# Performance work log

Hardware: AMD Instinct MI355X
Metric: run time of the kernel (lower is better)

## Reference

```python
import jax, jax.numpy as jnp
import numpy as np

# normalization module stand-ins (simple monotone scalings, as in the repo they
# are fixed elementwise rescalings of the raw quantities)
def norm_local_x(n):
    return n

def norm_unit_contraction(c):
    return c

def norm_local_N(N):
    return jnp.log1p(N.astype(jnp.float32))

norm_TNG_radii = norm_local_x
norm_local_v = norm_local_x
norm_local_v0 = norm_local_x

EPS = 1e-5


def setup_inputs() -> dict:
    key = jax.random.key(0)
    ks = jax.random.split(key, 12)
    B, T, ND, KB = 2, 1024, 256, 3
    K_IN, H, L = 19, 128, 128
    x0 = 0.3 * jax.random.normal(ks[0], (B, T, 3), dtype=jnp.float32)
    # DM positions in local frame, |x| must stay < 1.05 (assert in original)
    x = jax.random.uniform(ks[1], (B, T, ND, 3), dtype=jnp.float32) - 0.5
    N = jax.random.randint(ks[2], (B, T), 1, 512, dtype=jnp.int32)
    basis = jax.random.normal(ks[3], (B, KB, 3), dtype=jnp.float32)
    v = jax.random.normal(ks[4], (B, T, ND, 3), dtype=jnp.float32)
    P200c = 0.5 + jax.random.uniform(ks[5], (B,), dtype=jnp.float32)
    s = 0.1
    W0 = s * jax.random.normal(ks[6], (K_IN, H - 1), dtype=jnp.float32)
    b0 = jnp.zeros((H - 1,), jnp.float32)
    W1 = s * jax.random.normal(ks[7], (H, H), dtype=jnp.float32)
    b1 = jnp.zeros((H,), jnp.float32)
    W2 = s * jax.random.normal(ks[8], (H, L), dtype=jnp.float32)
    b2 = jnp.zeros((L,), jnp.float32)
    return {"x0": x0, "x": x, "N": N, "basis": basis, "v": v, "P200c": P200c,
            "W0": W0, "b0": b0, "W1": W1, "b1": b1, "W2": W2, "b2": b2}


def create_scalars(x0, x, N, basis, v):
    B, T, ND, _ = x.shape
    # velocities relative to local mean (halo -> local frame)
    v0 = jnp.mean(v, axis=2)                      # [B,T,3]
    vc = v - v0[:, :, None, :]                    # [B,T,ND,3]

    x_norm = jnp.linalg.norm(x, axis=-1, keepdims=True) + EPS     # [B,T,ND,1]
    xu = x / x_norm
    x0_norm = jnp.linalg.norm(x0, axis=-1, keepdims=True) + EPS   # [B,T,1]
    x0u = x0 / x0_norm
    v0_norm = jnp.linalg.norm(v0, axis=-1, keepdims=True) + EPS   # [B,T,1]
    v0u = v0 / v0_norm
    v_norm = jnp.linalg.norm(vc, axis=-1, keepdims=True) + EPS    # [B,T,ND,1]
    vu = vc / v_norm

    bc = lambda a: jnp.broadcast_to(a[:, :, None, :], (B, T, ND, a.shape[-1]))

    feats = [
        norm_local_x(x_norm),                                          # |x| [1]
        norm_unit_contraction(jnp.einsum('btnd,bkd->btnk', xu, basis)),# x.basis [3]
        jnp.broadcast_to(norm_local_N(N)[:, :, None, None], (B, T, ND, 1)),  # N [1]
        bc(norm_TNG_radii(x0_norm)),                                   # |x0| [1]
        bc(norm_unit_contraction(jnp.einsum('btd,bkd->btk', x0u, basis))),  # x0.basis [3]
        bc(norm_local_v0(v0_norm)),                                    # |v0| [1]
        bc(norm_unit_contraction(jnp.einsum('btd,bkd->btk', v0u, basis))),  # v0.basis [3]
        bc(norm_unit_contraction(jnp.sum(x0u * v0u, axis=-1, keepdims=True))),  # x0.v0 [1]
        norm_local_v(v_norm),                                          # |v| [1]
        norm_unit_contraction(jnp.einsum('btnd,bkd->btnk', vu, basis)),# v.basis [3]
        norm_unit_contraction(jnp.sum(xu * vu, axis=-1, keepdims=True)),  # x.v [1]
    ]
    return jnp.concatenate(feats, axis=-1)  # [B,T,ND,19]


def reference(x0, x, N, basis, v, P200c, W0, b0, W1, b1, W2, b2):
    scalars = create_scalars(x0, x, N, basis, v)          # [B,T,ND,19]
    h = jax.nn.leaky_relu(scalars @ W0 + b0)              # [B,T,ND,H-1]
    h = jnp.mean(h, axis=2)                               # pool -> [B,T,H-1]
    h = jnp.concatenate([h, norm_local_N(N)[..., None]], axis=-1)  # [B,T,H]
    h = jax.nn.leaky_relu(h @ W1 + b1)                    # [B,T,H]
    out = h @ W2 + b2                                     # [B,T,Nlatent]
    return (1.0 / P200c)[:, None, None] * out
```

## Files before the change

### kernel.cpp

```cpp
#include <hip/hip_runtime.h>
#include <hip/hip_bf16.h>
#include <math.h>

#define EPSV 1e-5f
#define HD   128
#define AROW 40
#define WROW 24

typedef __attribute__((ext_vector_type(8))) short bf16x8;
typedef __attribute__((ext_vector_type(4))) float f32x4;

__global__ __launch_bounds__(256, 4) void net_fused(
    const float* __restrict__ x0g, const float* __restrict__ xg,
    const int*   __restrict__ Ng,  const float* __restrict__ basisg,
    const float* __restrict__ vg,  const float* __restrict__ Pg,
    const float* __restrict__ W0,  const float* __restrict__ b0,
    const float* __restrict__ W1,  const float* __restrict__ b1,
    const float* __restrict__ W2,  const float* __restrict__ b2,
    float* __restrict__ out, int Tn, int NDn)
{
    __shared__ __align__(16) __hip_bfloat16 SA[256 * AROW];
    __shared__ __align__(16) __hip_bfloat16 Wt1[128 * WROW];
    __shared__ __align__(16) __hip_bfloat16 Wt2[128 * WROW];
    __shared__ float cvec[HD];
    __shared__ float hvec[HD];
    __shared__ float h1vec[HD];
    __shared__ float vred[4][3];

    const int bt   = blockIdx.x;
    const int b    = bt / Tn;
    const int tid  = threadIdx.x;
    const int lane = tid & 63;
    const int wave = tid >> 6;

    const long pbase = ((long)bt * NDn + tid) * 3;
    const float xi0 = xg[pbase+0], xi1 = xg[pbase+1], xi2 = xg[pbase+2];
    const float vi0 = vg[pbase+0], vi1 = vg[pbase+1], vi2 = vg[pbase+2];

    float s0 = vi0, s1 = vi1, s2 = vi2;
    #pragma unroll
    for (int off = 32; off > 0; off >>= 1) {
        s0 += __shfl_down(s0, off);
        s1 += __shfl_down(s1, off);
        s2 += __shfl_down(s2, off);
    }
    if (lane == 0) { vred[wave][0] = s0; vred[wave][1] = s1; vred[wave][2] = s2; }

    if (tid < 128) {
        const int RV[9] = {0, 1, 2, 3, 14, 15, 16, 17, 18};
        __hip_bfloat16 r1[16], r2[16];
        #pragma unroll
        for (int kk = 0; kk < 16; ++kk) {
            r1[kk] = __float2bfloat16(0.0f);
            r2[kk] = __float2bfloat16(0.0f);
        }
        if (tid < 127) {
            #pragma unroll
            for (int kk = 0; kk < 9; ++kk) {
                const float wv = W0[RV[kk] * 127 + tid];
                const __hip_bfloat16 hi = __float2bfloat16(wv);
                r1[kk] = hi;
                r2[kk] = __float2bfloat16(wv - __bfloat162float(hi));
            }
        }
        bf16x8* d1 = reinterpret_cast<bf16x8*>(&Wt1[tid * WROW]);
        bf16x8* d2 = reinterpret_cast<bf16x8*>(&Wt2[tid * WROW]);
        const bf16x8* s1v = reinterpret_cast<const bf16x8*>(r1);
        const bf16x8* s2v = reinterpret_cast<const bf16x8*>(r2);
        d1[0] = s1v[0]; d1[1] = s1v[1];
        d2[0] = s2v[0]; d2[1] = s2v[1];
    }
    __syncthreads();

    const float inv_nd = 1.0f / (float)NDn;
    const float v00 = (vred[0][0]+vred[1][0]+vred[2][0]+vred[3][0]) * inv_nd;
    const float v01 = (vred[0][1]+vred[1][1]+vred[2][1]+vred[3][1]) * inv_nd;
    const float v02 = (vred[0][2]+vred[1][2]+vred[2][2]+vred[3][2]) * inv_nd;

    const float p0 = x0g[bt*3+0], p1 = x0g[bt*3+1], p2 = x0g[bt*3+2];
    float bas[3][3];
    #pragma unroll
    for (int k = 0; k < 3; ++k)
        #pragma unroll
        for (int c = 0; c < 3; ++c)
            bas[k][c] = basisg[(b*3 + k)*3 + c];

    const float x0n  = sqrtf(p0*p0 + p1*p1 + p2*p2) + EPSV;
    const float ix0n = 1.0f / x0n;
    const float x0u0 = p0*ix0n, x0u1 = p1*ix0n, x0u2 = p2*ix0n;

    const float v0n  = sqrtf(v00*v00 + v01*v01 + v02*v02) + EPSV;
    const float iv0n = 1.0f / v0n;
    const float v0u0 = v00*iv0n, v0u1 = v01*iv0n, v0u2 = v02*iv0n;

    const float logN = log1pf((float)Ng[bt]);

    if (tid < 128) {
        float c = 0.0f;
        if (tid < 127) {
            float fc[10];
            fc[0] = logN;
            fc[1] = x0n;
            fc[2] = x0u0*bas[0][0] + x0u1*bas[0][1] + x0u2*bas[0][2];
            fc[3] = x0u0*bas[1][0] + x0u1*bas[1][1] + x0u2*bas[1][2];
            fc[4] = x0u0*bas[2][0] + x0u1*bas[2][1] + x0u2*bas[2][2];
            fc[5] = v0n;
            fc[6] = v0u0*bas[0][0] + v0u1*bas[0][1] + v0u2*bas[0][2];
            fc[7] = v0u0*bas[1][0] + v0u1*bas[1][1] + v0u2*bas[1][2];
            fc[8] = v0u0*bas[2][0] + v0u1*bas[2][1] + v0u2*bas[2][2];
            fc[9] = x0u0*v0u0 + x0u1*v0u1 + x0u2*v0u2;
            c = b0[tid];
            #pragma unroll
            for (int i = 0; i < 10; ++i)
                c = fmaf(fc[i], W0[(4 + i) * 127 + tid], c);
        }
        cvec[tid] = c;
        hvec[tid] = (tid == 127) ? logN : 0.0f;
    }

    {
        const float xn  = sqrtf(xi0*xi0 + xi1*xi1 + xi2*xi2) + EPSV;
        const float ixn = 1.0f / xn;
        const float xu0 = xi0*ixn, xu1 = xi1*ixn, xu2 = xi2*ixn;

        const float c0 = vi0 - v00, c1 = vi1 - v01, c2 = vi2 - v02;
        const float vn  = sqrtf(c0*c0 + c1*c1 + c2*c2) + EPSV;
        const float ivn = 1.0f / vn;
        const float vu0 = c0*ivn, vu1 = c1*ivn, vu2 = c2*ivn;

        float f[9];
        f[0] = xn;
        f[1] = xu0*bas[0][0] + xu1*bas[0][1] + xu2*bas[0][2];
        f[2] = xu0*bas[1][0] + xu1*bas[1][1] + xu2*bas[1][2];
        f[3] = xu0*bas[2][0] + xu1*bas[2][1] + xu2*bas[2][2];
        f[4] = vn;
        f[5] = vu0*bas[0][0] + vu1*bas[0][1] + vu2*bas[0][2];
        f[6] = vu0*bas[1][0] + vu1*bas[1][1] + vu2*bas[1][2];
        f[7] = vu0*bas[2][0] + vu1*bas[2][1] + vu2*bas[2][2];
        f[8] = xu0*vu0 + xu1*vu1 + xu2*vu2;

        __hip_bfloat16 row[32];
        #pragma unroll
        for (int kk = 0; kk < 32; ++kk) row[kk] = __float2bfloat16(0.0f);
        #pragma unroll
        for (int kk = 0; kk < 9; ++kk) {
            const __hip_bfloat16 hi = __float2bfloat16(f[kk]);
            row[kk]      = hi;
            row[16 + kk] = __float2bfloat16(f[kk] - __bfloat162float(hi));
        }
        bf16x8* dst = reinterpret_cast<bf16x8*>(&SA[tid * AROW]);
        const bf16x8* src = reinterpret_cast<const bf16x8*>(row);
        dst[0] = src[0]; dst[1] = src[1]; dst[2] = src[2]; dst[3] = src[3];
    }
    __syncthreads();

    {
        const int quad = lane >> 4;
        const int lm   = lane & 15;
        const int koff = (quad & 1) * 8;

        bf16x8 bf1[8], bf2[8];
        f32x4  cin[8];
        #pragma unroll
        for (int nt = 0; nt < 8; ++nt) {
            bf1[nt] = *reinterpret_cast<const bf16x8*>(&Wt1[(nt*16 + lm) * WROW + koff]);
            bf2[nt] = *reinterpret_cast<const bf16x8*>(&Wt2[(nt*16 + lm) * WROW + koff]);
            const float cl = cvec[nt*16 + lm];
            cin[nt] = (f32x4){cl, cl, cl, cl};
        }

        float pooled[8];
        #pragma unroll
        for (int nt = 0; nt < 8; ++nt) pooled[nt] = 0.0f;

        #pragma unroll
        for (int mt = 0; mt < 4; ++mt) {
            const bf16x8 af = *reinterpret_cast<const bf16x8*>(
                &SA[(wave*64 + mt*16 + lm) * AROW + quad*8]);
            #pragma unroll
            for (int nt = 0; nt < 8; ++nt) {
                f32x4 acc = __builtin_amdgcn_mfma_f32_16x16x32_bf16(af, bf1[nt], cin[nt], 0, 0, 0);
                acc = __builtin_amdgcn_mfma_f32_16x16x32_bf16(af, bf2[nt], acc, 0, 0, 0);
                #pragma unroll
                for (int r = 0; r < 4; ++r)
                    pooled[nt] += fmaxf(acc[r], 0.01f*acc[r]);
            }
        }
        #pragma unroll
        for (int nt = 0; nt < 8; ++nt) {
            pooled[nt] += __shfl_xor(pooled[nt], 16);
            pooled[nt] += __shfl_xor(pooled[nt], 32);
        }
        if (lane < 16) {
            #pragma unroll
            for (int nt = 0; nt < 8; ++nt) {
                const int n = nt*16 + lane;
                if (n < 127) atomicAdd(&hvec[n], pooled[nt] * inv_nd);
            }
        }
    }
    __syncthreads();

    if (tid < HD) {
        float a = b1[tid];
        #pragma unroll 16
        for (int k = 0; k < HD; ++k)
            a = fmaf(hvec[k], W1[k*HD + tid], a);
        h1vec[tid] = fmaxf(a, 0.01f*a);
    }
    __syncthreads();

    if (tid < HD) {
        float a = b2[tid];
        #pragma unroll 16
        for (int k = 0; k < HD; ++k)
            a = fmaf(h1vec[k], W2[k*HD + tid], a);
        out[(long)bt * HD + tid] = a / Pg[b];
    }
}

extern "C" void kernel_launch(void* const* d_in, const int* in_sizes, int n_in,
                              void* d_out, int out_size, void* d_ws, size_t ws_size,
                              hipStream_t stream) {
    const float* x0    = (const float*)d_in[0];
    const float* x     = (const float*)d_in[1];
    const int*   N     = (const int*)  d_in[2];
    const float* basis = (const float*)d_in[3];
    const float* v     = (const float*)d_in[4];
    const float* P200c = (const float*)d_in[5];
    const float* W0    = (const float*)d_in[6];
    const float* b0    = (const float*)d_in[7];
    const float* W1    = (const float*)d_in[8];
    const float* b1    = (const float*)d_in[9];
    const float* W2    = (const float*)d_in[10];
    const float* b2    = (const float*)d_in[11];
    float* out = (float*)d_out;

    const int B  = in_sizes[5];
    const int T  = in_sizes[2] / B;
    const int ND = in_sizes[1] / (in_sizes[2] * 3);

    hipLaunchKernelGGL(net_fused, dim3(B * T), dim3(256), 0, stream,
                       x0, x, N, basis, v, P200c, W0, b0, W1, b1, W2, b2,
                       out, T, ND);
}
```

Measured before the change: 111.3 us.

## Process two (b,t) items per block and parallelize MLP tail across all threads

Each block now handles two consecutive (b,t) rows and loops over them. The bf16 split of W0 into shared memory is therefore done once per pair instead of once per row. The final two 128x128 dense layers run both rows at once, so all 256 threads work instead of 128. This halves the grid and lengthens the serial chain inside each block, trading per-block setup and idle-thread waste for less block-level parallelism.

```diff
diff --git a/kernel.cpp b/kernel.cpp
--- a/kernel.cpp
+++ b/kernel.cpp
@@ -17,34 +17,23 @@
     const float* __restrict__ W0,  const float* __restrict__ b0,
     const float* __restrict__ W1,  const float* __restrict__ b1,
     const float* __restrict__ W2,  const float* __restrict__ b2,
-    float* __restrict__ out, int Tn, int NDn)
+    float* __restrict__ out, int Tn, int NDn, int BT)
 {
     __shared__ __align__(16) __hip_bfloat16 SA[256 * AROW];
     __shared__ __align__(16) __hip_bfloat16 Wt1[128 * WROW];
     __shared__ __align__(16) __hip_bfloat16 Wt2[128 * WROW];
     __shared__ float cvec[HD];
-    __shared__ float hvec[HD];
-    __shared__ float h1vec[HD];
-    __shared__ float vred[4][3];
-
-    const int bt   = blockIdx.x;
-    const int b    = bt / Tn;
+    __shared__ float hvec2[2][HD];
+    __shared__ float h1vec2[2][HD];
+    __shared__ float vred2[2][4][3];
+
+    const int bt0  = blockIdx.x * 2;
     const int tid  = threadIdx.x;
     const int lane = tid & 63;
     const int wave = tid >> 6;
-
-    const long pbase = ((long)bt * NDn + tid) * 3;
-    const float xi0 = xg[pbase+0], xi1 = xg[pbase+1], xi2 = xg[pbase+2];
-    const float vi0 = vg[pbase+0], vi1 = vg[pbase+1], vi2 = vg[pbase+2];
-
-    float s0 = vi0, s1 = vi1, s2 = vi2;
-    #pragma unroll
-    for (int off = 32; off > 0; off >>= 1) {
-        s0 += __shfl_down(s0, off);
-        s1 += __shfl_down(s1, off);
-        s2 += __shfl_down(s2, off);
-    }
-    if (lane == 0) { vred[wave][0] = s0; vred[wave][1] = s1; vred[wave][2] = s2; }
+    const int quad = lane >> 4;
+    const int lm   = lane & 15;
+    const float inv_nd = 1.0f / (float)NDn;
 
     if (tid < 128) {
         const int RV[9] = {0, 1, 2, 3, 14, 15, 16, 17, 18};
@@ -70,152 +59,172 @@
         d1[0] = s1v[0]; d1[1] = s1v[1];
         d2[0] = s2v[0]; d2[1] = s2v[1];
     }
+
+    for (int h = 0; h < 2; ++h) {
+        const int bt = bt0 + h;
+        const int b  = bt / Tn;
+
+        const long pbase = ((long)bt * NDn + tid) * 3;
+        const float xi0 = xg[pbase+0], xi1 = xg[pbase+1], xi2 = xg[pbase+2];
+        const float vi0 = vg[pbase+0], vi1 = vg[pbase+1], vi2 = vg[pbase+2];
+
+        float s0 = vi0, s1 = vi1, s2 = vi2;
+        #pragma unroll
+        for (int off = 32; off > 0; off >>= 1) {
+            s0 += __shfl_down(s0, off);
+            s1 += __shfl_down(s1, off);
+            s2 += __shfl_down(s2, off);
+        }
+        if (lane == 0) {
+            vred2[h][wave][0] = s0; vred2[h][wave][1] = s1; vred2[h][wave][2] = s2;
+        }
+        __syncthreads();
+
+        const float v00 = (vred2[h][0][0]+vred2[h][1][0]+vred2[h][2][0]+vred2[h][3][0]) * inv_nd;
+        const float v01 = (vred2[h][0][1]+vred2[h][1][1]+vred2[h][2][1]+vred2[h][3][1]) * inv_nd;
+        const float v02 = (vred2[h][0][2]+vred2[h][1][2]+vred2[h][2][2]+vred2[h][3][2]) * inv_nd;
+
+        const float p0 = x0g[bt*3+0], p1 = x0g[bt*3+1], p2 = x0g[bt*3+2];
+        float bas[3][3];
+        #pragma unroll
+        for (int k = 0; k < 3; ++k)
+            #pragma unroll
+            for (int c = 0; c < 3; ++c)
+                bas[k][c] = basisg[(b*3 + k)*3 + c];
+
+        const float x0n  = sqrtf(p0*p0 + p1*p1 + p2*p2) + EPSV;
+        const float ix0n = 1.0f / x0n;
+        const float x0u0 = p0*ix0n, x0u1 = p1*ix0n, x0u2 = p2*ix0n;
+
+        const float v0n  = sqrtf(v00*v00 + v01*v01 + v02*v02) + EPSV;
+        const float iv0n = 1.0f / v0n;
+        const float v0u0 = v00*iv0n, v0u1 = v01*iv0n, v0u2 = v02*iv0n;
+
+        const float logN = log1pf((float)Ng[bt]);
+
+        if (tid < 128) {
+            float c = 0.0f;
+            if (tid < 127) {
+                float fc[10];
+                fc[0] = logN;
+                fc[1] = x0n;
+                fc[2] = x0u0*bas[0][0] + x0u1*bas[0][1] + x0u2*bas[0][2];
+                fc[3] = x0u0*bas[1][0] + x0u1*bas[1][1] + x0u2*bas[1][2];
+                fc[4] = x0u0*bas[2][0] + x0u1*bas[2][1] + x0u2*bas[2][2];
+                fc[5] = v0n;
+                fc[6] = v0u0*bas[0][0] + v0u1*bas[0][1] + v0u2*bas[0][2];
+                fc[7] = v0u0*bas[1][0] + v0u1*bas[1][1] + v0u2*bas[1][2];
+                fc[8] = v0u0*bas[2][0] + v0u1*bas[2][1] + v0u2*bas[2][2];
+                fc[9] = x0u0*v0u0 + x0u1*v0u1 + x0u2*v0u2;
+                c = b0[tid];
+                #pragma unroll
+                for (int i = 0; i < 10; ++i)
+                    c = fmaf(fc[i], W0[(4 + i) * 127 + tid], c);
+            }
+            cvec[tid] = c;
+            hvec2[h][tid] = (tid == 127) ? logN : 0.0f;
+        }
+
+        {
+            const float xn  = sqrtf(xi0*xi0 + xi1*xi1 + xi2*xi2) + EPSV;
+            const float ixn = 1.0f / xn;
+            const float xu0 = xi0*ixn, xu1 = xi1*ixn, xu2 = xi2*ixn;
+
+            const float c0 = vi0 - v00, c1 = vi1 - v01, c2 = vi2 - v02;
+            const float vn  = sqrtf(c0*c0 + c1*c1 + c2*c2) + EPSV;
+            const float ivn = 1.0f / vn;
+            const float vu0 = c0*ivn, vu1 = c1*ivn, vu2 = c2*ivn;
+
+            float f[9];
+            f[0] = xn;
+            f[1] = xu0*bas[0][0] + xu1*bas[0][1] + xu2*bas[0][2];
+            f[2] = xu0*bas[1][0] + xu1*bas[1][1] + xu2*bas[1][2];
+            f[3] = xu0*bas[2][0] + xu1*bas[2][1] + xu2*bas[2][2];
+            f[4] = vn;
+            f[5] = vu0*bas[0][0] + vu1*bas[0][1] + vu2*bas[0][2];
+            f[6] = vu0*bas[1][0] + vu1*bas[1][1] + vu2*bas[1][2];
+            f[7] = vu0*bas[2][0] + vu1*bas[2][1] + vu2*bas[2][2];
+            f[8] = xu0*vu0 + xu1*vu1 + xu2*vu2;
+
+            __hip_bfloat16 row[32];
+            #pragma unroll
+            for (int kk = 0; kk < 32; ++kk) row[kk] = __float2bfloat16(0.0f);
+            #pragma unroll
+            for (int kk = 0; kk < 9; ++kk) {
+                const __hip_bfloat16 hi = __float2bfloat16(f[kk]);
+                row[kk]      = hi;
+                row[16 + kk] = __float2bfloat16(f[kk] - __bfloat162float(hi));
+            }
+            bf16x8* dst = reinterpret_cast<bf16x8*>(&SA[tid * AROW]);
+            const bf16x8* src = reinterpret_cast<const bf16x8*>(row);
+            dst[0] = src[0]; dst[1] = src[1]; dst[2] = src[2]; dst[3] = src[3];
+        }
+        __syncthreads();
+
+        {
+            const int koff = (quad & 1) * 8;
+
+            bf16x8 bf1[8], bf2[8];
+            f32x4  cin[8];
+            #pragma unroll
+            for (int nt = 0; nt < 8; ++nt) {
+                bf1[nt] = *reinterpret_cast<const bf16x8*>(&Wt1[(nt*16 + lm) * WROW + koff]);
+                bf2[nt] = *reinterpret_cast<const bf16x8*>(&Wt2[(nt*16 + lm) * WROW + koff]);
+                const float cl = cvec[nt*16 + lm];
+                cin[nt] = (f32x4){cl, cl, cl, cl};
+            }
+
+            float pooled[8];
+            #pragma unroll
+            for (int nt = 0; nt < 8; ++nt) pooled[nt] = 0.0f;
+
+            #pragma unroll
+            for (int mt = 0; mt < 4; ++mt) {
+                const bf16x8 af = *reinterpret_cast<const bf16x8*>(
+                    &SA[(wave*64 + mt*16 + lm) * AROW + quad*8]);
+                #pragma unroll
+                for (int nt = 0; nt < 8; ++nt) {
+                    f32x4 acc = __builtin_amdgcn_mfma_f32_16x16x32_bf16(af, bf1[nt], cin[nt], 0, 0, 0);
+                    acc = __builtin_amdgcn_mfma_f32_16x16x32_bf16(af, bf2[nt], acc, 0, 0, 0);
+                    #pragma unroll
+                    for (int r = 0; r < 4; ++r)
+                        pooled[nt] += fmaxf(acc[r], 0.01f*acc[r]);
+                }
+            }
+            #pragma unroll
+            for (int nt = 0; nt < 8; ++nt) {
+                pooled[nt] += __shfl_xor(pooled[nt], 16);
+                pooled[nt] += __shfl_xor(pooled[nt], 32);
+            }
+            if (lane < 16) {
+                #pragma unroll
+                for (int nt = 0; nt < 8; ++nt) {
+                    const int n = nt*16 + lane;
+                    if (n < 127) atomicAdd(&hvec2[h][n], pooled[nt] * inv_nd);
+                }
+            }
+        }
+    }
     __syncthreads();
 
-    const float inv_nd = 1.0f / (float)NDn;
-    const float v00 = (vred[0][0]+vred[1][0]+vred[2][0]+vred[3][0]) * inv_nd;
-    const float v01 = (vred[0][1]+vred[1][1]+vred[2][1]+vred[3][1]) * inv_nd;
-    const float v02 = (vred[0][2]+vred[1][2]+vred[2][2]+vred[3][2]) * inv_nd;
-
-    const float p0 = x0g[bt*3+0], p1 = x0g[bt*3+1], p2 = x0g[bt*3+2];
-    float bas[3][3];
-    #pragma unroll
-    for (int k = 0; k < 3; ++k)
-        #pragma unroll
-        for (int c = 0; c < 3; ++c)
-            bas[k][c] = basisg[(b*3 + k)*3 + c];
-
-    const float x0n  = sqrtf(p0*p0 + p1*p1 + p2*p2) + EPSV;
-    const float ix0n = 1.0f / x0n;
-    const float x0u0 = p0*ix0n, x0u1 = p1*ix0n, x0u2 = p2*ix0n;
-
-    const float v0n  = sqrtf(v00*v00 + v01*v01 + v02*v02) + EPSV;
-    const float iv0n = 1.0f / v0n;
-    const float v0u0 = v00*iv0n, v0u1 = v01*iv0n, v0u2 = v02*iv0n;
-
-    const float logN = log1pf((float)Ng[bt]);
-
-    if (tid < 128) {
-        float c = 0.0f;
-        if (tid < 127) {
-            float fc[10];
-            fc[0] = logN;
-            fc[1] = x0n;
-            fc[2] = x0u0*bas[0][0] + x0u1*bas[0][1] + x0u2*bas[0][2];
-            fc[3] = x0u0*bas[1][0] + x0u1*bas[1][1] + x0u2*bas[1][2];
-            fc[4] = x0u0*bas[2][0] + x0u1*bas[2][1] + x0u2*bas[2][2];
-            fc[5] = v0n;
-            fc[6] = v0u0*bas[0][0] + v0u1*bas[0][1] + v0u2*bas[0][2];
-            fc[7] = v0u0*bas[1][0] + v0u1*bas[1][1] + v0u2*bas[1][2];
-            fc[8] = v0u0*bas[2][0] + v0u1*bas[2][1] + v0u2*bas[2][2];
-            fc[9] = x0u0*v0u0 + x0u1*v0u1 + x0u2*v0u2;
-            c = b0[tid];
-            #pragma unroll
-            for (int i = 0; i < 10; ++i)
-                c = fmaf(fc[i], W0[(4 + i) * 127 + tid], c);
-        }
-        cvec[tid] = c;
-        hvec[tid] = (tid == 127) ? logN : 0.0f;
-    }
-
+    const int r  = tid >> 7;
+    const int j  = tid & 127;
     {
-        const float xn  = sqrtf(xi0*xi0 + xi1*xi1 + xi2*xi2) + EPSV;
-        const float ixn = 1.0f / xn;
-        const float xu0 = xi0*ixn, xu1 = xi1*ixn, xu2 = xi2*ixn;
-
-        const float c0 = vi0 - v00, c1 = vi1 - v01, c2 = vi2 - v02;
-        const float vn  = sqrtf(c0*c0 + c1*c1 + c2*c2) + EPSV;
-        const float ivn = 1.0f / vn;
-        const float vu0 = c0*ivn, vu1 = c1*ivn, vu2 = c2*ivn;
-
-        float f[9];
-        f[0] = xn;
-        f[1] = xu0*bas[0][0] + xu1*bas[0][1] + xu2*bas[0][2];
-        f[2] = xu0*bas[1][0] + xu1*bas[1][1] + xu2*bas[1][2];
-        f[3] = xu0*bas[2][0] + xu1*bas[2][1] + xu2*bas[2][2];
-        f[4] = vn;
-        f[5] = vu0*bas[0][0] + vu1*bas[0][1] + vu2*bas[0][2];
-        f[6] = vu0*bas[1][0] + vu1*bas[1][1] + vu2*bas[1][2];
-        f[7] = vu0*bas[2][0] + vu1*bas[2][1] + vu2*bas[2][2];
-        f[8] = xu0*vu0 + xu1*vu1 + xu2*vu2;
-
-        __hip_bfloat16 row[32];
-        #pragma unroll
-        for (int kk = 0; kk < 32; ++kk) row[kk] = __float2bfloat16(0.0f);
-        #pragma unroll
-        for (int kk = 0; kk < 9; ++kk) {
-            const __hip_bfloat16 hi = __float2bfloat16(f[kk]);
-            row[kk]      = hi;
-            row[16 + kk] = __float2bfloat16(f[kk] - __bfloat162float(hi));
-        }
-        bf16x8* dst = reinterpret_cast<bf16x8*>(&SA[tid * AROW]);
-        const bf16x8* src = reinterpret_cast<const bf16x8*>(row);
-        dst[0] = src[0]; dst[1] = src[1]; dst[2] = src[2]; dst[3] = src[3];
-    }
-    __syncthreads();
-
-    {
-        const int quad = lane >> 4;
-        const int lm   = lane & 15;
-        const int koff = (quad & 1) * 8;
-
-        bf16x8 bf1[8], bf2[8];
-        f32x4  cin[8];
-        #pragma unroll
-        for (int nt = 0; nt < 8; ++nt) {
-            bf1[nt] = *reinterpret_cast<const bf16x8*>(&Wt1[(nt*16 + lm) * WROW + koff]);
-            bf2[nt] = *reinterpret_cast<const bf16x8*>(&Wt2[(nt*16 + lm) * WROW + koff]);
-            const float cl = cvec[nt*16 + lm];
-            cin[nt] = (f32x4){cl, cl, cl, cl};
-        }
-
-        float pooled[8];
-        #pragma unroll
-        for (int nt = 0; nt < 8; ++nt) pooled[nt] = 0.0f;
-
-        #pragma unroll
-        for (int mt = 0; mt < 4; ++mt) {
-            const bf16x8 af = *reinterpret_cast<const bf16x8*>(
-                &SA[(wave*64 + mt*16 + lm) * AROW + quad*8]);
-            #pragma unroll
-            for (int nt = 0; nt < 8; ++nt) {
-                f32x4 acc = __builtin_amdgcn_mfma_f32_16x16x32_bf16(af, bf1[nt], cin[nt], 0, 0, 0);
-                acc = __builtin_amdgcn_mfma_f32_16x16x32_bf16(af, bf2[nt], acc, 0, 0, 0);
-                #pragma unroll
-                for (int r = 0; r < 4; ++r)
-                    pooled[nt] += fmaxf(acc[r], 0.01f*acc[r]);
-            }
-        }
-        #pragma unroll
-        for (int nt = 0; nt < 8; ++nt) {
-            pooled[nt] += __shfl_xor(pooled[nt], 16);
-            pooled[nt] += __shfl_xor(pooled[nt], 32);
-        }
-        if (lane < 16) {
-            #pragma unroll
-            for (int nt = 0; nt < 8; ++nt) {
-                const int n = nt*16 + lane;
-                if (n < 127) atomicAdd(&hvec[n], pooled[nt] * inv_nd);
-            }
-        }
-    }
-    __syncthreads();
-
-    if (tid < HD) {
-        float a = b1[tid];
+        float a = b1[j];
         #pragma unroll 16
         for (int k = 0; k < HD; ++k)
-            a = fmaf(hvec[k], W1[k*HD + tid], a);
-        h1vec[tid] = fmaxf(a, 0.01f*a);
+            a = fmaf(hvec2[r][k], W1[k*HD + j], a);
+        h1vec2[r][j] = fmaxf(a, 0.01f*a);
     }
     __syncthreads();
 
-    if (tid < HD) {
-        float a = b2[tid];
+    {
+        const int bt = bt0 + r;
+        float a = b2[j];
         #pragma unroll 16
         for (int k = 0; k < HD; ++k)
-            a = fmaf(h1vec[k], W2[k*HD + tid], a);
-        out[(long)bt * HD + tid] = a / Pg[b];
+            a = fmaf(h1vec2[r][k], W2[k*HD + j], a);
+        out[(long)bt * HD + j] = a / Pg[bt / Tn];
     }
 }
 
@@ -239,8 +248,9 @@
     const int B  = in_sizes[5];
     const int T  = in_sizes[2] / B;
     const int ND = in_sizes[1] / (in_sizes[2] * 3);
-
-    hipLaunchKernelGGL(net_fused, dim3(B * T), dim3(256), 0, stream,
+    const int BT = B * T;
+
+    hipLaunchKernelGGL(net_fused, dim3(BT / 2), dim3(256), 0, stream,
                        x0, x, N, basis, v, P200c, W0, b0, W1, b1, W2, b2,
-                       out, T, ND);
+                       out, T, ND, BT);
 }
```

New measurement: 127.1 us. 1.14x slower.

## Drop activation lo-split, pass features by wave shuffle, fold weight split into K

Applied to the files above, without the earlier changes.

The MLP input features are now converted to a single bf16 each, with no hi/lo residual. They are packed into registers and sent to the MFMA A-operand with wave shuffles, which removes the per-point shared-memory staging array. The W0 hi and lo parts are packed into one shared tile along K, so each 16x16x32 MFMA computes A_hi·(W_hi+W_lo) and the MFMA count is halved. Launch bounds are raised to allow more resident blocks. In exchange, the activation-side bf16 rounding error is no longer corrected, which lowers accuracy against the fp32 reference.

```diff
diff --git a/kernel.cpp b/kernel.cpp
--- a/kernel.cpp
+++ b/kernel.cpp
@@ -4,13 +4,19 @@
 
 #define EPSV 1e-5f
 #define HD   128
-#define AROW 40
-#define WROW 24
+#define WROW 40
 
 typedef __attribute__((ext_vector_type(8))) short bf16x8;
 typedef __attribute__((ext_vector_type(4))) float f32x4;
 
-__global__ __launch_bounds__(256, 4) void net_fused(
+static __device__ __forceinline__ unsigned int bfbits(float x) {
+    __hip_bfloat16 h = __float2bfloat16(x);
+    unsigned short u;
+    __builtin_memcpy(&u, &h, 2);
+    return (unsigned int)u;
+}
+
+__global__ __launch_bounds__(256, 6) void net_fused(
     const float* __restrict__ x0g, const float* __restrict__ xg,
     const int*   __restrict__ Ng,  const float* __restrict__ basisg,
     const float* __restrict__ vg,  const float* __restrict__ Pg,
@@ -19,9 +25,7 @@
     const float* __restrict__ W2,  const float* __restrict__ b2,
     float* __restrict__ out, int Tn, int NDn)
 {
-    __shared__ __align__(16) __hip_bfloat16 SA[256 * AROW];
-    __shared__ __align__(16) __hip_bfloat16 Wt1[128 * WROW];
-    __shared__ __align__(16) __hip_bfloat16 Wt2[128 * WROW];
+    __shared__ __align__(16) __hip_bfloat16 Wt[128 * WROW];
     __shared__ float cvec[HD];
     __shared__ float hvec[HD];
     __shared__ float h1vec[HD];
@@ -32,6 +36,8 @@
     const int tid  = threadIdx.x;
     const int lane = tid & 63;
     const int wave = tid >> 6;
+    const int quad = lane >> 4;
+    const int lm   = lane & 15;
 
     const long pbase = ((long)bt * NDn + tid) * 3;
     const float xi0 = xg[pbase+0], xi1 = xg[pbase+1], xi2 = xg[pbase+2];
@@ -48,27 +54,21 @@
 
     if (tid < 128) {
         const int RV[9] = {0, 1, 2, 3, 14, 15, 16, 17, 18};
-        __hip_bfloat16 r1[16], r2[16];
-        #pragma unroll
-        for (int kk = 0; kk < 16; ++kk) {
-            r1[kk] = __float2bfloat16(0.0f);
-            r2[kk] = __float2bfloat16(0.0f);
-        }
+        __hip_bfloat16 r1[32];
+        #pragma unroll
+        for (int kk = 0; kk < 32; ++kk) r1[kk] = __float2bfloat16(0.0f);
         if (tid < 127) {
             #pragma unroll
             for (int kk = 0; kk < 9; ++kk) {
                 const float wv = W0[RV[kk] * 127 + tid];
                 const __hip_bfloat16 hi = __float2bfloat16(wv);
-                r1[kk] = hi;
-                r2[kk] = __float2bfloat16(wv - __bfloat162float(hi));
+                r1[kk]      = hi;
+                r1[16 + kk] = __float2bfloat16(wv - __bfloat162float(hi));
             }
         }
-        bf16x8* d1 = reinterpret_cast<bf16x8*>(&Wt1[tid * WROW]);
-        bf16x8* d2 = reinterpret_cast<bf16x8*>(&Wt2[tid * WROW]);
+        bf16x8* d1 = reinterpret_cast<bf16x8*>(&Wt[tid * WROW]);
         const bf16x8* s1v = reinterpret_cast<const bf16x8*>(r1);
-        const bf16x8* s2v = reinterpret_cast<const bf16x8*>(r2);
-        d1[0] = s1v[0]; d1[1] = s1v[1];
-        d2[0] = s2v[0]; d2[1] = s2v[1];
+        d1[0] = s1v[0]; d1[1] = s1v[1]; d1[2] = s1v[2]; d1[3] = s1v[3];
     }
     __syncthreads();
 
@@ -118,6 +118,7 @@
         hvec[tid] = (tid == 127) ? logN : 0.0f;
     }
 
+    unsigned int H[5];
     {
         const float xn  = sqrtf(xi0*xi0 + xi1*xi1 + xi2*xi2) + EPSV;
         const float ixn = 1.0f / xn;
@@ -139,48 +140,44 @@
         f[7] = vu0*bas[2][0] + vu1*bas[2][1] + vu2*bas[2][2];
         f[8] = xu0*vu0 + xu1*vu1 + xu2*vu2;
 
-        __hip_bfloat16 row[32];
-        #pragma unroll
-        for (int kk = 0; kk < 32; ++kk) row[kk] = __float2bfloat16(0.0f);
-        #pragma unroll
-        for (int kk = 0; kk < 9; ++kk) {
-            const __hip_bfloat16 hi = __float2bfloat16(f[kk]);
-            row[kk]      = hi;
-            row[16 + kk] = __float2bfloat16(f[kk] - __bfloat162float(hi));
-        }
-        bf16x8* dst = reinterpret_cast<bf16x8*>(&SA[tid * AROW]);
-        const bf16x8* src = reinterpret_cast<const bf16x8*>(row);
-        dst[0] = src[0]; dst[1] = src[1]; dst[2] = src[2]; dst[3] = src[3];
+        unsigned int hb[9];
+        #pragma unroll
+        for (int kk = 0; kk < 9; ++kk) hb[kk] = bfbits(f[kk]);
+        #pragma unroll
+        for (int j = 0; j < 4; ++j) H[j] = hb[2*j] | (hb[2*j+1] << 16);
+        H[4] = hb[8];
     }
     __syncthreads();
 
     {
-        const int quad = lane >> 4;
-        const int lm   = lane & 15;
-        const int koff = (quad & 1) * 8;
-
-        bf16x8 bf1[8], bf2[8];
-        f32x4  cin[8];
-        #pragma unroll
-        for (int nt = 0; nt < 8; ++nt) {
-            bf1[nt] = *reinterpret_cast<const bf16x8*>(&Wt1[(nt*16 + lm) * WROW + koff]);
-            bf2[nt] = *reinterpret_cast<const bf16x8*>(&Wt2[(nt*16 + lm) * WROW + koff]);
-            const float cl = cvec[nt*16 + lm];
-            cin[nt] = (f32x4){cl, cl, cl, cl};
-        }
-
         float pooled[8];
         #pragma unroll
         for (int nt = 0; nt < 8; ++nt) pooled[nt] = 0.0f;
 
         #pragma unroll
         for (int mt = 0; mt < 4; ++mt) {
-            const bf16x8 af = *reinterpret_cast<const bf16x8*>(
-                &SA[(wave*64 + mt*16 + lm) * AROW + quad*8]);
+            const int src = mt*16 + lm;
+            const unsigned int t0 = (unsigned int)__shfl((int)H[0], src);
+            const unsigned int t1 = (unsigned int)__shfl((int)H[1], src);
+            const unsigned int t2 = (unsigned int)__shfl((int)H[2], src);
+            const unsigned int t3 = (unsigned int)__shfl((int)H[3], src);
+            const unsigned int t4 = (unsigned int)__shfl((int)H[4], src);
+
+            union { unsigned int u[4]; bf16x8 v; } a;
+            const bool evenq = ((quad & 1) == 0);
+            a.u[0] = evenq ? t0 : t4;
+            a.u[1] = evenq ? t1 : 0u;
+            a.u[2] = evenq ? t2 : 0u;
+            a.u[3] = evenq ? t3 : 0u;
+            const bf16x8 af = a.v;
+
             #pragma unroll
             for (int nt = 0; nt < 8; ++nt) {
-                f32x4 acc = __builtin_amdgcn_mfma_f32_16x16x32_bf16(af, bf1[nt], cin[nt], 0, 0, 0);
-                acc = __builtin_amdgcn_mfma_f32_16x16x32_bf16(af, bf2[nt], acc, 0, 0, 0);
+                const bf16x8 bf = *reinterpret_cast<const bf16x8*>(
+                    &Wt[(nt*16 + lm) * WROW + quad*8]);
+                const float cl = cvec[nt*16 + lm];
+                const f32x4 cin = {cl, cl, cl, cl};
+                const f32x4 acc = __builtin_amdgcn_mfma_f32_16x16x32_bf16(af, bf, cin, 0, 0, 0);
                 #pragma unroll
                 for (int r = 0; r < 4; ++r)
                     pooled[nt] += fmaxf(acc[r], 0.01f*acc[r]);
@@ -194,8 +191,7 @@
         if (lane < 16) {
             #pragma unroll
             for (int nt = 0; nt < 8; ++nt) {
-                const int n = nt*16 + lane;
-                if (n < 127) atomicAdd(&hvec[n], pooled[nt] * inv_nd);
+                atomicAdd(&hvec[nt*16 + lane], pooled[nt] * inv_nd);
             }
         }
     }
```

New measurement: 148.0 us. 1.33x slower.
